# Kernel tuning notes

Measured on AMD Instinct MI355X. Metric: run time of the kernel, lower is better.

Reference implementation:

```python
import jax, jax.numpy as jnp
import numpy as np

N_NODES = 50000
N_EDGES = 800000
IN_DIM, HID, HEADS = 3, 64, 4
NEG_SLOPE = 0.2  # PyG GATConv default leaky_relu slope


def _glorot(key, shape):
    fan_in, fan_out = shape[0], shape[-1]
    lim = (6.0 / (fan_in + fan_out)) ** 0.5
    return jax.random.uniform(key, shape, jnp.float32, -lim, lim)


def setup_inputs() -> dict:
    key = jax.random.key(0)
    ks = jax.random.split(key, 12)
    x = jax.random.normal(ks[0], (N_NODES, IN_DIM), jnp.float32)
    edge_index = jax.random.randint(ks[1], (2, N_EDGES), 0, N_NODES, jnp.int64)
    return {
        "x": x,
        "edge_index": edge_index,
        "W1": _glorot(ks[2], (IN_DIM, HEADS * HID)),
        "a_src1": _glorot(ks[3], (HEADS, HID)),
        "a_dst1": _glorot(ks[4], (HEADS, HID)),
        "b1": jnp.zeros((HEADS * HID,), jnp.float32),
        "W2": _glorot(ks[5], (HEADS * HID, HID)),
        "a_src2": _glorot(ks[6], (1, HID)),
        "a_dst2": _glorot(ks[7], (1, HID)),
        "b2": jnp.zeros((HID,), jnp.float32),
        # fc: 64 -> 1
        "Wfc": _glorot(ks[8], (HID, 1)),
        "bfc": jnp.zeros((1,), jnp.float32),
    }


def _gat_layer(x, src, dst, W, a_src, a_dst, b, heads, out_ch, n):
    # h: [N, H, C]
    h = (x @ W).reshape(n, heads, out_ch)
    # per-node attention halves, gathered per edge -> [E, H]
    alpha_s = jnp.einsum("nhc,hc->nh", h, a_src)
    alpha_d = jnp.einsum("nhc,hc->nh", h, a_dst)
    e = jax.nn.leaky_relu(alpha_s[src] + alpha_d[dst], NEG_SLOPE)
    # numerically stable segment softmax over incoming edges of each dst node
    e_max = jax.ops.segment_max(e, dst, num_segments=n)
    ex = jnp.exp(e - e_max[dst])
    denom = jax.ops.segment_sum(ex, dst, num_segments=n)
    alpha = ex / (denom[dst] + 1e-16)  # [E, H]
    # weighted scatter-aggregate of source features
    msg = h[src] * alpha[:, :, None]  # [E, H, C]
    out = jax.ops.segment_sum(msg, dst, num_segments=n)  # [N, H, C]
    return out.reshape(n, heads * out_ch) + b


def reference(x, edge_index, W1, a_src1, a_dst1, b1, W2, a_src2, a_dst2, b2, Wfc, bfc):
    n = x.shape[0]
    # PyG GATConv adds self-loops by default
    loops = jnp.arange(n, dtype=edge_index.dtype)
    src = jnp.concatenate([edge_index[0], loops])
    dst = jnp.concatenate([edge_index[1], loops])
    # dropout layers are identity in eval mode
    h = _gat_layer(x, src, dst, W1, a_src1, a_dst1, b1, HEADS, HID, n)
    h = jax.nn.elu(h)
    h = _gat_layer(h, src, dst, W2, a_src2, a_dst2, b2, 1, HID, n)
    h = jax.nn.elu(h)
    out = jax.nn.sigmoid(h @ Wfc + bfc)
    return out.squeeze(-1)
```

## Files before the change

### kernel.cpp

```cpp
#include <hip/hip_runtime.h>
#include <hip/hip_fp16.h>
#include <math.h>

#define N_NODES 50000
#define N_EDGES 800000
#define E_TOT   (N_EDGES + N_NODES)
#define NEG_SLOPE 0.2f
#define NSLICE 8
#define NODES_PER_SLICE (N_NODES / NSLICE)
#define SLICE_BLOCKS 256

#define CNT_OFF    0UL
#define CSR_OFF    200000UL
#define VAS2_OFF   6600000UL
#define VAD2_OFF   6601024UL
#define PK1_OFF    6602048UL
#define AD1_OFF    8202048UL
#define H2_OFF     9002048UL
#define AS2_OFF    15402048UL
#define AD2_OFF    15602048UL

__device__ __forceinline__ float wave_reduce_sum(float v) {
    #pragma unroll
    for (int off = 32; off > 0; off >>= 1) v += __shfl_xor(v, off, 64);
    return v;
}
__device__ __forceinline__ float grp_reduce_sum(float v) {
    #pragma unroll
    for (int off = 8; off > 0; off >>= 1) v += __shfl_xor(v, off, 64);
    return v;
}
__device__ __forceinline__ float lrelu(float v) { return v > 0.f ? v : NEG_SLOPE * v; }
__device__ __forceinline__ float elu(float v)   { return v > 0.f ? v : __expf(v) - 1.f; }

__global__ void node_alpha1(const float* __restrict__ x, const float* __restrict__ W1,
                            const float* __restrict__ a_s1, const float* __restrict__ a_d1,
                            const float* __restrict__ W2, const float* __restrict__ a_s2,
                            const float* __restrict__ a_d2,
                            float* __restrict__ pk1, float* __restrict__ ad1,
                            unsigned* __restrict__ cnt,
                            float* __restrict__ vas2, float* __restrict__ vad2) {
    __shared__ float svs[12], svd[12];
    int t = threadIdx.x, h = t >> 6, lane = t & 63;
    float avs = a_s1[h*64 + lane], avd = a_d1[h*64 + lane];
    #pragma unroll
    for (int k = 0; k < 3; ++k) {
        float w = W1[k*256 + h*64 + lane];
        float ps = wave_reduce_sum(w * avs);
        float pd = wave_reduce_sum(w * avd);
        if (lane == 0) { svs[k*4+h] = ps; svd[k*4+h] = pd; }
    }
    if (blockIdx.x < 64) {
        int k = blockIdx.x*4 + h;
        float wv = W2[k*64 + lane];
        float ps2 = wave_reduce_sum(wv * a_s2[lane]);
        float pd2 = wave_reduce_sum(wv * a_d2[lane]);
        if (lane == 0) { vas2[k] = ps2; vad2[k] = pd2; }
    }
    __syncthreads();
    int n = blockIdx.x*256 + t;
    if (n >= N_NODES) return;
    cnt[n] = 0u;
    float x0 = x[n*3+0], x1 = x[n*3+1], x2v = x[n*3+2];
    float4 s, d;
    s.x = x0*svs[0] + x1*svs[4] + x2v*svs[8];
    s.y = x0*svs[1] + x1*svs[5] + x2v*svs[9];
    s.z = x0*svs[2] + x1*svs[6] + x2v*svs[10];
    s.w = x0*svs[3] + x1*svs[7] + x2v*svs[11];
    d.x = x0*svd[0] + x1*svd[4] + x2v*svd[8];
    d.y = x0*svd[1] + x1*svd[5] + x2v*svd[9];
    d.z = x0*svd[2] + x1*svd[6] + x2v*svd[10];
    d.w = x0*svd[3] + x1*svd[7] + x2v*svd[11];
    float4* pp = (float4*)(pk1 + (size_t)n*8);
    pp[0] = s;
    pp[1] = make_float4(x0, x1, x2v, 0.f);
    *(float4*)(ad1 + (size_t)n*4) = d;
}

__global__ void build_csr(const int* __restrict__ ei, unsigned* __restrict__ cnt,
                          unsigned short* __restrict__ csr) {
    int slice = blockIdx.x & (NSLICE-1);
    int bi    = blockIdx.x >> 3;
    int lo = slice * NODES_PER_SLICE, hi = lo + NODES_PER_SLICE;
    const int stride = SLICE_BLOCKS * 256;
    for (int c = bi*256 + threadIdx.x; c < N_EDGES/4; c += stride) {
        int4 d4 = *(const int4*)(ei + N_EDGES + c*4);
        if (d4.x >= lo && d4.x < hi) {
            unsigned p = atomicAdd(&cnt[d4.x], 1u);
            if (p < 64u) csr[((size_t)d4.x << 6) + p] = (unsigned short)ei[c*4+0];
        }
        if (d4.y >= lo && d4.y < hi) {
            unsigned p = atomicAdd(&cnt[d4.y], 1u);
            if (p < 64u) csr[((size_t)d4.y << 6) + p] = (unsigned short)ei[c*4+1];
        }
        if (d4.z >= lo && d4.z < hi) {
            unsigned p = atomicAdd(&cnt[d4.z], 1u);
            if (p < 64u) csr[((size_t)d4.z << 6) + p] = (unsigned short)ei[c*4+2];
        }
        if (d4.w >= lo && d4.w < hi) {
            unsigned p = atomicAdd(&cnt[d4.w], 1u);
            if (p < 64u) csr[((size_t)d4.w << 6) + p] = (unsigned short)ei[c*4+3];
        }
    }
    for (int v = lo + bi*256 + threadIdx.x; v < hi; v += stride) {
        unsigned p = atomicAdd(&cnt[v], 1u);
        if (p < 64u) csr[((size_t)v << 6) + p] = (unsigned short)v;
    }
}

#define KB 32
__global__ __launch_bounds__(256) void layer1_fused(
        const unsigned short* __restrict__ csr, const unsigned* __restrict__ cnt,
        const float* __restrict__ pk1, const float* __restrict__ ad1,
        const float* __restrict__ W1, const float* __restrict__ b1,
        const float* __restrict__ W2,
        const float* __restrict__ vas2, const float* __restrict__ vad2,
        __half* __restrict__ h2, float* __restrict__ as2, float* __restrict__ ad2) {
    __shared__ float gl[64][12];
    __shared__ float xT[KB][68];
    __shared__ float Wt[KB][64];
    __shared__ float W1s[768], b1s[256];
    int t = threadIdx.x;
    W1s[t] = W1[t]; W1s[256+t] = W1[256+t]; W1s[512+t] = W1[512+t];
    b1s[t] = b1[t];
    int n0 = blockIdx.x * 64;
    int subl = t & 15, ng = t >> 4;
    #pragma unroll
    for (int pass = 0; pass < 4; ++pass) {
        int li = pass*16 + ng;
        int n = n0 + li;
        float d0=0.f, d1=0.f, d2=0.f, d3=0.f;
        float g00=0,g01=0,g02=0, g10=0,g11=0,g12=0, g20=0,g21=0,g22=0, g30=0,g31=0,g32=0;
        if (n < N_NODES) {
            unsigned deg = min(cnt[n], 64u);
            const unsigned short* row = csr + ((size_t)n << 6);
            float4 adv = *(const float4*)(ad1 + (size_t)n*4);
            for (unsigned c = subl; c < deg; c += 16) {
                int s = row[c];
                const float4* pp = (const float4*)(pk1 + (size_t)s*8);
                float4 as = pp[0];
                float4 xv = pp[1];
                float e0 = __expf(lrelu(as.x+adv.x));
                float e1 = __expf(lrelu(as.y+adv.y));
                float e2 = __expf(lrelu(as.z+adv.z));
                float e3 = __expf(lrelu(as.w+adv.w));
                d0 += e0; d1 += e1; d2 += e2; d3 += e3;
                g00 = fmaf(e0,xv.x,g00); g01 = fmaf(e0,xv.y,g01); g02 = fmaf(e0,xv.z,g02);
                g10 = fmaf(e1,xv.x,g10); g11 = fmaf(e1,xv.y,g11); g12 = fmaf(e1,xv.z,g12);
                g20 = fmaf(e2,xv.x,g20); g21 = fmaf(e2,xv.y,g21); g22 = fmaf(e2,xv.z,g22);
                g30 = fmaf(e3,xv.x,g30); g31 = fmaf(e3,xv.y,g31); g32 = fmaf(e3,xv.z,g32);
            }
        }
        float r_0 = 1.f/(grp_reduce_sum(d0) + 1e-16f);
        float r_1 = 1.f/(grp_reduce_sum(d1) + 1e-16f);
        float r_2 = 1.f/(grp_reduce_sum(d2) + 1e-16f);
        float r_3 = 1.f/(grp_reduce_sum(d3) + 1e-16f);
        g00 = grp_reduce_sum(g00)*r_0; g01 = grp_reduce_sum(g01)*r_0; g02 = grp_reduce_sum(g02)*r_0;
        g10 = grp_reduce_sum(g10)*r_1; g11 = grp_reduce_sum(g11)*r_1; g12 = grp_reduce_sum(g12)*r_1;
        g20 = grp_reduce_sum(g20)*r_2; g21 = grp_reduce_sum(g21)*r_2; g22 = grp_reduce_sum(g22)*r_2;
        g30 = grp_reduce_sum(g30)*r_3; g31 = grp_reduce_sum(g31)*r_3; g32 = grp_reduce_sum(g32)*r_3;
        if (subl == 0) {
            float* gp = &gl[li][0];
            *(float4*)(gp+0) = make_float4(g00, g01, g02, g10);
            *(float4*)(gp+4) = make_float4(g11, g12, g20, g21);
            *(float4*)(gp+8) = make_float4(g22, g30, g31, g32);
        }
    }
    __syncthreads();
    int i = t & 15, j = t >> 4;
    int snode = t >> 2, g8 = t & 3;
    float acc[4][4] = {{0,0,0,0},{0,0,0,0},{0,0,0,0},{0,0,0,0}};
    float pas = 0.f, pad = 0.f;
    for (int k0 = 0; k0 < 256; k0 += KB) {
        __syncthreads();
        {
            int h = k0 >> 6;
            float gv0 = gl[snode][h*3+0];
            float gv1 = gl[snode][h*3+1];
            float gv2 = gl[snode][h*3+2];
            int jbase = k0 + g8*8;
            #pragma unroll
            for (int q = 0; q < 8; ++q) {
                int jj = jbase + q;
                float val = gv0*W1s[jj] + gv1*W1s[256+jj] + gv2*W1s[512+jj] + b1s[jj];
                val = elu(val);
                xT[jj - k0][snode] = val;
                pas = fmaf(val, vas2[jj], pas);
                pad = fmaf(val, vad2[jj], pad);
            }
        }
        int p = t;
        #pragma unroll
        for (int rr = 0; rr < 2; ++rr, p += 256) {
            int kr = p >> 4, c4 = p & 15;
            *(float4*)(&Wt[kr][c4*4]) = *(const float4*)(W2 + (size_t)(k0+kr)*64 + c4*4);
        }
        __syncthreads();
        #pragma unroll
        for (int k = 0; k < KB; ++k) {
            float4 xv = *(const float4*)(&xT[k][4*i]);
            float4 wv = *(const float4*)(&Wt[k][4*j]);
            acc[0][0]=fmaf(xv.x,wv.x,acc[0][0]); acc[0][1]=fmaf(xv.x,wv.y,acc[0][1]);
            acc[0][2]=fmaf(xv.x,wv.z,acc[0][2]); acc[0][3]=fmaf(xv.x,wv.w,acc[0][3]);
            acc[1][0]=fmaf(xv.y,wv.x,acc[1][0]); acc[1][1]=fmaf(xv.y,wv.y,acc[1][1]);
            acc[1][2]=fmaf(xv.y,wv.z,acc[1][2]); acc[1][3]=fmaf(xv.y,wv.w,acc[1][3]);
            acc[2][0]=fmaf(xv.z,wv.x,acc[2][0]); acc[2][1]=fmaf(xv.z,wv.y,acc[2][1]);
            acc[2][2]=fmaf(xv.z,wv.z,acc[2][2]); acc[2][3]=fmaf(xv.z,wv.w,acc[2][3]);
            acc[3][0]=fmaf(xv.w,wv.x,acc[3][0]); acc[3][1]=fmaf(xv.w,wv.y,acc[3][1]);
            acc[3][2]=fmaf(xv.w,wv.z,acc[3][2]); acc[3][3]=fmaf(xv.w,wv.w,acc[3][3]);
        }
    }
    pas += __shfl_xor(pas, 1, 64); pas += __shfl_xor(pas, 2, 64);
    pad += __shfl_xor(pad, 1, 64); pad += __shfl_xor(pad, 2, 64);
    if (g8 == 0 && n0 + snode < N_NODES) { as2[n0+snode] = pas; ad2[n0+snode] = pad; }
    #pragma unroll
    for (int ii = 0; ii < 4; ++ii) {
        int n = n0 + 4*i + ii;
        if (n < N_NODES) {
            union { __half2 h[2]; float2 f; } u;
            u.h[0] = __floats2half2_rn(acc[ii][0], acc[ii][1]);
            u.h[1] = __floats2half2_rn(acc[ii][2], acc[ii][3]);
            *(float2*)(h2 + (size_t)n*64 + 4*j) = u.f;
        }
    }
}

__global__ void gat2_node(const unsigned short* __restrict__ csr, const unsigned* __restrict__ cnt,
                          const __half* __restrict__ h2, const float* __restrict__ as2,
                          const float* __restrict__ ad2, const float* __restrict__ b2,
                          const float* __restrict__ Wfc, const float* __restrict__ bfc,
                          float* __restrict__ out) {
    int lane = threadIdx.x & 63, w = threadIdx.x >> 6;
    int n = blockIdx.x*4 + w;
    unsigned deg = min(cnt[n], 64u);
    const unsigned short* row = csr + ((size_t)n << 6);
    float adv = ad2[n];
    int s_l = 0; float ex_l = 0.f;
    if (lane < (int)deg) {
        s_l = row[lane];
        ex_l = __expf(lrelu(as2[s_l] + adv));
    }
    float den = wave_reduce_sum(ex_l);
    float acc = 0.f;
    unsigned degr = (deg + 7u) & ~7u;
    for (unsigned c = 0; c < degr; c += 8) {
        #pragma unroll
        for (int u = 0; u < 8; ++u) {
            int e = (int)c + u;
            float ex = __shfl(ex_l, e, 64);
            int   s  = __shfl(s_l,  e, 64);
            float hv = __half2float(h2[((size_t)s << 6) + lane]);
            acc = fmaf(hv, ex, acc);
        }
    }
    float v = elu(acc/(den + 1e-16f) + b2[lane]);
    float part = wave_reduce_sum(v * Wfc[lane]);
    if (lane == 0) out[n] = 1.f/(1.f + __expf(-(part + bfc[0])));
}

extern "C" void kernel_launch(void* const* d_in, const int* in_sizes, int n_in,
                              void* d_out, int out_size, void* d_ws, size_t ws_size,
                              hipStream_t stream) {
    const float* x      = (const float*)d_in[0];
    const int*   ei     = (const int*)  d_in[1];
    const float* W1     = (const float*)d_in[2];
    const float* a_src1 = (const float*)d_in[3];
    const float* a_dst1 = (const float*)d_in[4];
    const float* b1     = (const float*)d_in[5];
    const float* W2     = (const float*)d_in[6];
    const float* a_src2 = (const float*)d_in[7];
    const float* a_dst2 = (const float*)d_in[8];
    const float* b2     = (const float*)d_in[9];
    const float* Wfc    = (const float*)d_in[10];
    const float* bfc    = (const float*)d_in[11];
    float* out = (float*)d_out;

    char* ws = (char*)d_ws;
    unsigned*       cnt  = (unsigned*)      (ws + CNT_OFF);
    unsigned short* csr  = (unsigned short*)(ws + CSR_OFF);
    float*          vas2 = (float*)         (ws + VAS2_OFF);
    float*          vad2 = (float*)         (ws + VAD2_OFF);
    float*          pk1  = (float*)         (ws + PK1_OFF);
    float*          ad1  = (float*)         (ws + AD1_OFF);
    __half*         h2   = (__half*)        (ws + H2_OFF);
    float*          as2  = (float*)         (ws + AS2_OFF);
    float*          ad2  = (float*)         (ws + AD2_OFF);

    const int BLK = 256;
    node_alpha1  <<<(N_NODES + BLK - 1)/BLK, BLK, 0, stream>>>(
        x, W1, a_src1, a_dst1, W2, a_src2, a_dst2, pk1, ad1, cnt, vas2, vad2);
    build_csr    <<<NSLICE*SLICE_BLOCKS, BLK, 0, stream>>>(ei, cnt, csr);
    layer1_fused <<<(N_NODES + 63)/64, BLK, 0, stream>>>(
        csr, cnt, pk1, ad1, W1, b1, W2, vas2, vad2, h2, as2, ad2);
    gat2_node    <<<N_NODES/4, BLK, 0, stream>>>(csr, cnt, h2, as2, ad2, b2, Wfc, bfc, out);
}
```

Baseline: 129.4 us.

## Halve nodes per block in layer1_fused to double grid parallelism

The fused layer-1 kernel now handles 32 nodes per block instead of 64, using 8 lanes per node for the edge gather in a single pass. The GEMM tile changes to 4 nodes by 2 output columns per thread, and the layer-2 attention partial sums are reduced through shared memory. The aim is to launch twice as many blocks for better occupancy and to shorten the serial gather passes, at the cost of reloading W1/W2 per block twice as often and doing less register reuse per thread in the GEMM.

```diff
diff --git a/kernel.cpp b/kernel.cpp
--- a/kernel.cpp
+++ b/kernel.cpp
@@ -25,9 +25,9 @@
     for (int off = 32; off > 0; off >>= 1) v += __shfl_xor(v, off, 64);
     return v;
 }
-__device__ __forceinline__ float grp_reduce_sum(float v) {
-    #pragma unroll
-    for (int off = 8; off > 0; off >>= 1) v += __shfl_xor(v, off, 64);
+__device__ __forceinline__ float grp8_reduce_sum(float v) {
+    #pragma unroll
+    for (int off = 4; off > 0; off >>= 1) v += __shfl_xor(v, off, 64);
     return v;
 }
 __device__ __forceinline__ float lrelu(float v) { return v > 0.f ? v : NEG_SLOPE * v; }
@@ -116,26 +116,25 @@
         const float* __restrict__ W2,
         const float* __restrict__ vas2, const float* __restrict__ vad2,
         __half* __restrict__ h2, float* __restrict__ as2, float* __restrict__ ad2) {
-    __shared__ float gl[64][12];
-    __shared__ float xT[KB][68];
+    __shared__ float gl[32][13];
+    __shared__ float xT[KB][36];
     __shared__ float Wt[KB][64];
     __shared__ float W1s[768], b1s[256];
+    __shared__ float pas_part[8][33], pad_part[8][33];
     int t = threadIdx.x;
     W1s[t] = W1[t]; W1s[256+t] = W1[256+t]; W1s[512+t] = W1[512+t];
     b1s[t] = b1[t];
-    int n0 = blockIdx.x * 64;
-    int subl = t & 15, ng = t >> 4;
-    #pragma unroll
-    for (int pass = 0; pass < 4; ++pass) {
-        int li = pass*16 + ng;
-        int n = n0 + li;
+    int n0 = blockIdx.x * 32;
+    {
+        int subl = t & 7, ng = t >> 3;
+        int n = n0 + ng;
         float d0=0.f, d1=0.f, d2=0.f, d3=0.f;
         float g00=0,g01=0,g02=0, g10=0,g11=0,g12=0, g20=0,g21=0,g22=0, g30=0,g31=0,g32=0;
         if (n < N_NODES) {
             unsigned deg = min(cnt[n], 64u);
             const unsigned short* row = csr + ((size_t)n << 6);
             float4 adv = *(const float4*)(ad1 + (size_t)n*4);
-            for (unsigned c = subl; c < deg; c += 16) {
+            for (unsigned c = subl; c < deg; c += 8) {
                 int s = row[c];
                 const float4* pp = (const float4*)(pk1 + (size_t)s*8);
                 float4 as = pp[0];
@@ -151,25 +150,25 @@
                 g30 = fmaf(e3,xv.x,g30); g31 = fmaf(e3,xv.y,g31); g32 = fmaf(e3,xv.z,g32);
             }
         }
-        float r_0 = 1.f/(grp_reduce_sum(d0) + 1e-16f);
-        float r_1 = 1.f/(grp_reduce_sum(d1) + 1e-16f);
-        float r_2 = 1.f/(grp_reduce_sum(d2) + 1e-16f);
-        float r_3 = 1.f/(grp_reduce_sum(d3) + 1e-16f);
-        g00 = grp_reduce_sum(g00)*r_0; g01 = grp_reduce_sum(g01)*r_0; g02 = grp_reduce_sum(g02)*r_0;
-        g10 = grp_reduce_sum(g10)*r_1; g11 = grp_reduce_sum(g11)*r_1; g12 = grp_reduce_sum(g12)*r_1;
-        g20 = grp_reduce_sum(g20)*r_2; g21 = grp_reduce_sum(g21)*r_2; g22 = grp_reduce_sum(g22)*r_2;
-        g30 = grp_reduce_sum(g30)*r_3; g31 = grp_reduce_sum(g31)*r_3; g32 = grp_reduce_sum(g32)*r_3;
+        float r_0 = 1.f/(grp8_reduce_sum(d0) + 1e-16f);
+        float r_1 = 1.f/(grp8_reduce_sum(d1) + 1e-16f);
+        float r_2 = 1.f/(grp8_reduce_sum(d2) + 1e-16f);
+        float r_3 = 1.f/(grp8_reduce_sum(d3) + 1e-16f);
+        g00 = grp8_reduce_sum(g00)*r_0; g01 = grp8_reduce_sum(g01)*r_0; g02 = grp8_reduce_sum(g02)*r_0;
+        g10 = grp8_reduce_sum(g10)*r_1; g11 = grp8_reduce_sum(g11)*r_1; g12 = grp8_reduce_sum(g12)*r_1;
+        g20 = grp8_reduce_sum(g20)*r_2; g21 = grp8_reduce_sum(g21)*r_2; g22 = grp8_reduce_sum(g22)*r_2;
+        g30 = grp8_reduce_sum(g30)*r_3; g31 = grp8_reduce_sum(g31)*r_3; g32 = grp8_reduce_sum(g32)*r_3;
         if (subl == 0) {
-            float* gp = &gl[li][0];
-            *(float4*)(gp+0) = make_float4(g00, g01, g02, g10);
-            *(float4*)(gp+4) = make_float4(g11, g12, g20, g21);
-            *(float4*)(gp+8) = make_float4(g22, g30, g31, g32);
+            gl[ng][0]=g00;  gl[ng][1]=g01;  gl[ng][2]=g02;
+            gl[ng][3]=g10;  gl[ng][4]=g11;  gl[ng][5]=g12;
+            gl[ng][6]=g20;  gl[ng][7]=g21;  gl[ng][8]=g22;
+            gl[ng][9]=g30;  gl[ng][10]=g31; gl[ng][11]=g32;
         }
     }
     __syncthreads();
-    int i = t & 15, j = t >> 4;
-    int snode = t >> 2, g8 = t & 3;
-    float acc[4][4] = {{0,0,0,0},{0,0,0,0},{0,0,0,0},{0,0,0,0}};
+    int i = t & 7, j = t >> 3;
+    int snode = t & 31, kw = t >> 5;
+    float acc[4][2] = {{0,0},{0,0},{0,0},{0,0}};
     float pas = 0.f, pad = 0.f;
     for (int k0 = 0; k0 < 256; k0 += KB) {
         __syncthreads();
@@ -178,13 +177,13 @@
             float gv0 = gl[snode][h*3+0];
             float gv1 = gl[snode][h*3+1];
             float gv2 = gl[snode][h*3+2];
-            int jbase = k0 + g8*8;
             #pragma unroll
-            for (int q = 0; q < 8; ++q) {
-                int jj = jbase + q;
+            for (int q = 0; q < 4; ++q) {
+                int k  = kw*4 + q;
+                int jj = k0 + k;
                 float val = gv0*W1s[jj] + gv1*W1s[256+jj] + gv2*W1s[512+jj] + b1s[jj];
                 val = elu(val);
-                xT[jj - k0][snode] = val;
+                xT[k][snode] = val;
                 pas = fmaf(val, vas2[jj], pas);
                 pad = fmaf(val, vad2[jj], pad);
             }
@@ -199,29 +198,30 @@
         #pragma unroll
         for (int k = 0; k < KB; ++k) {
             float4 xv = *(const float4*)(&xT[k][4*i]);
-            float4 wv = *(const float4*)(&Wt[k][4*j]);
+            float2 wv = *(const float2*)(&Wt[k][2*j]);
             acc[0][0]=fmaf(xv.x,wv.x,acc[0][0]); acc[0][1]=fmaf(xv.x,wv.y,acc[0][1]);
-            acc[0][2]=fmaf(xv.x,wv.z,acc[0][2]); acc[0][3]=fmaf(xv.x,wv.w,acc[0][3]);
             acc[1][0]=fmaf(xv.y,wv.x,acc[1][0]); acc[1][1]=fmaf(xv.y,wv.y,acc[1][1]);
-            acc[1][2]=fmaf(xv.y,wv.z,acc[1][2]); acc[1][3]=fmaf(xv.y,wv.w,acc[1][3]);
             acc[2][0]=fmaf(xv.z,wv.x,acc[2][0]); acc[2][1]=fmaf(xv.z,wv.y,acc[2][1]);
-            acc[2][2]=fmaf(xv.z,wv.z,acc[2][2]); acc[2][3]=fmaf(xv.z,wv.w,acc[2][3]);
             acc[3][0]=fmaf(xv.w,wv.x,acc[3][0]); acc[3][1]=fmaf(xv.w,wv.y,acc[3][1]);
-            acc[3][2]=fmaf(xv.w,wv.z,acc[3][2]); acc[3][3]=fmaf(xv.w,wv.w,acc[3][3]);
-        }
-    }
-    pas += __shfl_xor(pas, 1, 64); pas += __shfl_xor(pas, 2, 64);
-    pad += __shfl_xor(pad, 1, 64); pad += __shfl_xor(pad, 2, 64);
-    if (g8 == 0 && n0 + snode < N_NODES) { as2[n0+snode] = pas; ad2[n0+snode] = pad; }
+        }
+    }
+    pas_part[kw][snode] = pas;
+    pad_part[kw][snode] = pad;
+    __syncthreads();
+    if (t < 32) {
+        int n = n0 + t;
+        if (n < N_NODES) {
+            float s = 0.f, d = 0.f;
+            #pragma unroll
+            for (int m = 0; m < 8; ++m) { s += pas_part[m][t]; d += pad_part[m][t]; }
+            as2[n] = s; ad2[n] = d;
+        }
+    }
     #pragma unroll
     for (int ii = 0; ii < 4; ++ii) {
         int n = n0 + 4*i + ii;
-        if (n < N_NODES) {
-            union { __half2 h[2]; float2 f; } u;
-            u.h[0] = __floats2half2_rn(acc[ii][0], acc[ii][1]);
-            u.h[1] = __floats2half2_rn(acc[ii][2], acc[ii][3]);
-            *(float2*)(h2 + (size_t)n*64 + 4*j) = u.f;
-        }
+        if (n < N_NODES)
+            *(__half2*)(h2 + (size_t)n*64 + 2*j) = __floats2half2_rn(acc[ii][0], acc[ii][1]);
     }
 }
 
@@ -290,7 +290,7 @@
     node_alpha1  <<<(N_NODES + BLK - 1)/BLK, BLK, 0, stream>>>(
         x, W1, a_src1, a_dst1, W2, a_src2, a_dst2, pk1, ad1, cnt, vas2, vad2);
     build_csr    <<<NSLICE*SLICE_BLOCKS, BLK, 0, stream>>>(ei, cnt, csr);
-    layer1_fused <<<(N_NODES + 63)/64, BLK, 0, stream>>>(
+    layer1_fused <<<(N_NODES + 31)/32, BLK, 0, stream>>>(
         csr, cnt, pk1, ad1, W1, b1, W2, vas2, vad2, h2, as2, ad2);
     gat2_node    <<<N_NODES/4, BLK, 0, stream>>>(csr, cnt, h2, as2, ad2, b2, Wfc, bfc, out);
 }
```

Result: no change. 126.9 us (-1.9%).
